# Kernel optimization log

Measured on AMD Instinct MI355X. Metric: run time of the kernel, lower is better.

## Reference

```python
import jax, jax.numpy as jnp
import numpy as np

H = 128          # hidden_size
GRID = 4         # grid_dim
CELL = 0.5       # cell_size
PRED_LEN = 12
EMB = H // 4     # social pooling embed dim = 32


def setup_inputs() -> dict:
    key = jax.random.key(0)
    ks = jax.random.split(key, 13)
    B, N, T = 16384, 64, 8
    s = 0.05
    return {
        "obs": jax.random.normal(ks[0], (B, T, 2), jnp.float32),
        "neighbors": jax.random.normal(ks[1], (B, N, T, 2), jnp.float32),
        "embed_table": jax.random.normal(ks[2], (GRID * GRID + 1, EMB), jnp.float32) * s,
        "W_in": jax.random.normal(ks[3], (H, 2), jnp.float32) * s,
        "b_in": jax.random.normal(ks[4], (H,), jnp.float32) * s,
        "W_sp": jax.random.normal(ks[5], (H, EMB), jnp.float32) * s,
        "b_sp": jax.random.normal(ks[6], (H,), jnp.float32) * s,
        "W_ih": jax.random.normal(ks[7], (4 * H, 2 * H), jnp.float32) * s,
        "W_hh": jax.random.normal(ks[8], (4 * H, H), jnp.float32) * s,
        "b_ih": jax.random.normal(ks[9], (4 * H,), jnp.float32) * s,
        "b_hh": jax.random.normal(ks[10], (4 * H,), jnp.float32) * s,
        "W_out": jax.random.normal(ks[11], (2, H), jnp.float32) * s,
        "b_out": jax.random.normal(ks[12], (2,), jnp.float32) * s,
    }


def reference(obs, neighbors, embed_table, W_in, b_in, W_sp, b_sp,
              W_ih, W_hh, b_ih, b_hh, W_out, b_out):
    B = obs.shape[0]
    half = GRID // 2

    def pool(rel):  # rel: [B, N, 2] -> [B, EMB]
        idx = jnp.clip(jnp.floor(rel / CELL).astype(jnp.int32), -half, half - 1) + half
        # after clamp+shift, idx in [0, GRID-1], so index is always valid (matches torch path)
        flat = idx[..., 0] * GRID + idx[..., 1]  # [B, N]
        return embed_table[flat].sum(axis=1)     # sum-pool over neighbors

    def lstm(h, c, x):  # torch LSTMCell gate order: i, f, g, o
        gates = x @ W_ih.T + b_ih + h @ W_hh.T + b_hh  # [B, 4H]
        i, f, g, o = jnp.split(gates, 4, axis=-1)
        c2 = jax.nn.sigmoid(f) * c + jax.nn.sigmoid(i) * jnp.tanh(g)
        h2 = jax.nn.sigmoid(o) * jnp.tanh(c2)
        return h2, c2

    def obs_step(carry, xs):
        h, c = carry
        o_t, nb_t = xs  # [B,2], [B,N,2]
        agent = o_t @ W_in.T + b_in                        # [B,H]
        social = pool(nb_t - o_t[:, None, :]) @ W_sp.T + b_sp  # [B,H]
        h, c = lstm(h, c, jnp.concatenate([agent, social], axis=-1))
        return (h, c), None

    h0 = jnp.zeros((B, H), obs.dtype)
    c0 = jnp.zeros((B, H), obs.dtype)
    obs_tf = jnp.swapaxes(obs, 0, 1)          # [T,B,2]
    nb_tf = jnp.moveaxis(neighbors, 2, 0)     # [T,B,N,2]
    (h, c), _ = jax.lax.scan(obs_step, (h0, c0), (obs_tf, nb_tf))

    def pred_step(carry, _):
        h, c, prev = carry
        agent = prev @ W_in.T + b_in
        x = jnp.concatenate([agent, jnp.zeros_like(agent)], axis=-1)
        h, c = lstm(h, c, x)
        disp = h @ W_out.T + b_out  # [B,2]
        return (h, c, disp), disp

    prev0 = jnp.zeros((B, 2), obs.dtype)
    _, fut = jax.lax.scan(pred_step, (h, c, prev0), None, length=PRED_LEN)
    return jnp.swapaxes(fut, 0, 1)  # [B, PRED_LEN, 2]
```

## Files before the change

kernel.cpp:

```cpp
#include <hip/hip_runtime.h>
#include <math.h>

typedef _Float16 f16;
typedef f16 f16x8 __attribute__((ext_vector_type(8)));
typedef float f32x4 __attribute__((ext_vector_type(4)));

#define Bsz   16384
#define Tobs  8
#define PREDL 12
#define MR    32

__device__ __forceinline__ float fast_sigm(float x) {
  float e = __builtin_amdgcn_exp2f(-1.44269504f * x);
  return __builtin_amdgcn_rcpf(1.f + e);
}
__device__ __forceinline__ float fast_tanh(float x) {
  float e = __builtin_amdgcn_exp2f(2.88539008f * x);
  return 1.f - 2.f * __builtin_amdgcn_rcpf(1.f + e);
}

#define AB(buf, kt, mt, lane, j) (((((buf)*4 + (kt))*2 + (mt))*64 + (lane))*8 + (j))

#define WF(ktw, w, nt, lane) ((size_t)((((ktw)*8 + (w))*4 + (nt))*64 + (lane)) * 8)

__global__ void wsp_t_kernel(const float* __restrict__ W_sp, const float* __restrict__ table,
                             float* __restrict__ Wsp_t) {
  int gid = blockIdx.x * 256 + threadIdx.x;
  if (gid >= 16 * 128) return;
  int c = gid >> 7, m = gid & 127;
  float s = 0.f;
  for (int e = 0; e < 32; ++e) s += W_sp[m * 32 + e] * table[c * 32 + e];
  Wsp_t[c * 128 + m] = s;
}

__global__ __launch_bounds__(64) void pack_all(
    const float* __restrict__ W_ih, const float* __restrict__ W_hh,
    const float* __restrict__ W_in, const float* __restrict__ Wsp_t,
    const float* __restrict__ b_in, const float* __restrict__ b_sp,
    const float* __restrict__ b_ih, const float* __restrict__ b_hh,
    const float* __restrict__ W_out, const float* __restrict__ b_out,
    f16* __restrict__ Wfrag, float* __restrict__ biasO,
    float* __restrict__ biasP, float* __restrict__ biasPE) {
  const int blk = blockIdx.x;
  const int nt = blk >> 7, w = (blk >> 4) & 7, l = blk & 15;
  const int jo = nt * 128 + w * 16 + l;
  const int m = threadIdx.x;
  __shared__ float st[256];

  float a0 = W_ih[jo * 256 + m],        a1 = W_ih[jo * 256 + 64 + m];
  float s0 = W_ih[jo * 256 + 128 + m],  s1 = W_ih[jo * 256 + 192 + m];
  float hh0 = W_hh[jo * 128 + m],       hh1 = W_hh[jo * 128 + 64 + m];
  float bi0 = b_in[m], bi1 = b_in[64 + m];
  float bs0 = b_sp[m], bs1 = b_sp[64 + m];
  float wi00 = W_in[m * 2 + 0],        wi01 = W_in[m * 2 + 1];
  float wi10 = W_in[(64 + m) * 2 + 0], wi11 = W_in[(64 + m) * 2 + 1];
  float wo00 = W_out[m],       wo01 = W_out[64 + m];
  float wo10 = W_out[128 + m], wo11 = W_out[192 + m];

  auto red = [](float v) {
#pragma unroll
    for (int s = 1; s < 64; s <<= 1) v += __shfl_xor(v, s);
    return v;
  };

  float cells[16];
#pragma unroll
  for (int c = 0; c < 16; ++c)
    cells[c] = red(s0 * Wsp_t[c * 128 + m] + s1 * Wsp_t[c * 128 + 64 + m]);
  float wio0 = red(a0 * wi00 + a1 * wi10);
  float wio1 = red(a0 * wi01 + a1 * wi11);
  float dotA = red(a0 * bi0 + a1 * bi1);
  float dotS = red(s0 * bs0 + s1 * bs1);

  st[m] = hh0;
  st[64 + m] = hh1;
  st[128 + m] = hh0 + wio0 * wo00 + wio1 * wo10;
  st[192 + m] = hh1 + wio0 * wo01 + wio1 * wo11;
  __syncthreads();

  if (m < 32) {
    int u = m & 15, kt = u >> 2, q = u & 3;
    int which = m >> 4;
    int ktw = which ? kt + 5 : kt;
    f16x8 v;
#pragma unroll
    for (int j = 0; j < 8; ++j) v[j] = (f16)st[which * 128 + kt * 32 + q * 8 + j];
    *(f16x8*)(Wfrag + WF(ktw, w, nt, q * 16 + l)) = v;
  } else if (m < 36) {
    int q = m - 32;
    f16x8 v;
#pragma unroll
    for (int j = 0; j < 8; ++j) {
      int kk = q * 8 + j;
      float x = (kk < 16) ? cells[kk] : (kk == 16 ? wio0 : (kk == 17 ? wio1 : 0.f));
      v[j] = (f16)x;
    }
    *(f16x8*)(Wfrag + WF(4, w, nt, q * 16 + l)) = v;
  } else if (m == 36) {
    int col = w * 64 + nt * 16 + l;
    float base = b_ih[jo] + b_hh[jo];
    biasO[col] = base + dotA + dotS;
    float bp = base + dotA;
    biasP[col] = bp;
    biasPE[col] = bp + wio0 * b_out[0] + wio1 * b_out[1];
  }
}

__global__ __launch_bounds__(256) void pool_kernel(const float* __restrict__ obs,
                                                   const float* __restrict__ nb,
                                                   f16* __restrict__ cntx) {
  int tid = threadIdx.x;
  int wv = tid >> 6, ln = tid & 63;
  int b = blockIdx.x * 4 + wv;
  const float4* nb4 = (const float4*)(nb + (((size_t)b * 64 + ln) * 8) * 2);
  float4 n0 = nb4[0], n1 = nb4[1], n2 = nb4[2], n3 = nb4[3];
  const float4* ob4 = (const float4*)(obs + (size_t)b * 16);
  float4 o0 = ob4[0], o1 = ob4[1], o2 = ob4[2], o3 = ob4[3];
  float nxv[8] = {n0.x, n0.z, n1.x, n1.z, n2.x, n2.z, n3.x, n3.z};
  float nyv[8] = {n0.y, n0.w, n1.y, n1.w, n2.y, n2.w, n3.y, n3.w};
  float oxv[8] = {o0.x, o0.z, o1.x, o1.z, o2.x, o2.z, o3.x, o3.z};
  float oyv[8] = {o0.y, o0.w, o1.y, o1.w, o2.y, o2.w, o3.y, o3.w};
  int flat[8];
#pragma unroll
  for (int t = 0; t < 8; ++t) {
    float rx = nxv[t] - oxv[t], ry = nyv[t] - oyv[t];
    int ix = (int)floorf(rx + rx);
    int iy = (int)floorf(ry + ry);
    ix = min(max(ix, -2), 1);
    iy = min(max(iy, -2), 1);
    flat[t] = (ix + 2) * 4 + (iy + 2);
  }
  int cnt0 = 0, cnt1 = 0;
#pragma unroll
  for (int t = 0; t < 8; ++t) {
#pragma unroll
    for (int c = 0; c < 16; ++c) {
      int n = (int)__popcll(__ballot(flat[t] == c));
      if (t < 4) cnt0 = (ln == t * 16 + c) ? n : cnt0;
      else       cnt1 = (ln == (t - 4) * 16 + c) ? n : cnt1;
    }
  }
  int myT = ln >> 4, myC = ln & 15;
  size_t base = (size_t)b * 8;
  cntx[(base + myT) * 32 + myC] = (f16)cnt0;
  cntx[(base + myT + 4) * 32 + myC] = (f16)cnt1;
  if (ln < 8) {
    float ox2 = obs[base * 2 + ln * 2], oy2 = obs[base * 2 + ln * 2 + 1];
    cntx[(base + ln) * 32 + 16] = (f16)ox2;
    cntx[(base + ln) * 32 + 17] = (f16)oy2;
  }
}

__global__ __launch_bounds__(512, 2) void social_lstm_main(
    const f16* __restrict__ Wfrag, const float* __restrict__ biasO,
    const float* __restrict__ biasP, const float* __restrict__ biasPE,
    const f16* __restrict__ cntx, const float* __restrict__ W_out,
    const float* __restrict__ b_out, float* __restrict__ out) {
  __shared__ __align__(16) f16 Abuf[2 * 4 * 2 * 64 * 8];

  const int tid = threadIdx.x;
  const int w = tid >> 6, ln = tid & 63;
  const int q = ln >> 4, l = ln & 15;
  const int b0 = blockIdx.x * MR;

  for (int i = tid; i < 2048; i += 512) ((uint32_t*)Abuf)[i] = 0u;

  f16x8 Bh[4][4];
#pragma unroll
  for (int kt = 0; kt < 4; ++kt)
#pragma unroll
    for (int nt = 0; nt < 4; ++nt)
      Bh[kt][nt] = *(const f16x8*)(Wfrag + WF(kt, w, nt, ln));
  f16x8 Bx[4];
#pragma unroll
  for (int nt = 0; nt < 4; ++nt) Bx[nt] = *(const f16x8*)(Wfrag + WF(4, w, nt, ln));

  float creg[8];
#pragma unroll
  for (int i = 0; i < 8; ++i) creg[i] = 0.f;

  float bOr[4], bPr[4];
#pragma unroll
  for (int g = 0; g < 4; ++g) {
    bOr[g] = biasO[w * 64 + g * 16 + l];
    bPr[g] = biasP[w * 64 + g * 16 + l];
  }

  const int hc = w * 16 + l;
  const int aw_kt = hc >> 5, aw_quad = (hc >> 3) & 3, aw_j = l & 7;

  f32x4 acc[2][4];

  auto gemm_h = [&](int rb) {
#pragma unroll
    for (int kt = 0; kt < 4; ++kt) {
      f16x8 Af[2];
#pragma unroll
      for (int mt = 0; mt < 2; ++mt) Af[mt] = *(const f16x8*)(&Abuf[AB(rb, kt, mt, ln, 0)]);
#pragma unroll
      for (int mt = 0; mt < 2; ++mt)
#pragma unroll
        for (int nt = 0; nt < 4; ++nt)
          acc[mt][nt] =
              __builtin_amdgcn_mfma_f32_16x16x32_f16(Af[mt], Bh[kt][nt], acc[mt][nt], 0, 0, 0);
    }
  };

  auto epilogue = [&](const float* bq, int wbuf) {
#pragma unroll
    for (int mt = 0; mt < 2; ++mt) {
#pragma unroll
      for (int reg = 0; reg < 4; ++reg) {
        float p0 = acc[mt][0][reg] + bq[0];
        float p1 = acc[mt][1][reg] + bq[1];
        float p2 = acc[mt][2][reg] + bq[2];
        float p3 = acc[mt][3][reg] + bq[3];
        float iv = fast_sigm(p0), fv = fast_sigm(p1);
        float gv = fast_tanh(p2), ov = fast_sigm(p3);
        int ci = mt * 4 + reg;
        float c2 = fv * creg[ci] + iv * gv;
        creg[ci] = c2;
        float hv = ov * fast_tanh(c2);
        Abuf[AB(wbuf, aw_kt, mt, (q * 4 + reg) + 16 * aw_quad, aw_j)] = (f16)hv;
      }
    }
  };

#pragma unroll
  for (int t = 0; t < Tobs; ++t) {
    const int rb = t & 1, wb = rb ^ 1;
    __syncthreads();
    f16x8 Ax[2];
#pragma unroll
    for (int mt = 0; mt < 2; ++mt)
      Ax[mt] = *(const f16x8*)(cntx + ((size_t)(b0 + mt * 16 + l) * Tobs + t) * 32 + q * 8);
#pragma unroll
    for (int mt = 0; mt < 2; ++mt)
#pragma unroll
      for (int nt = 0; nt < 4; ++nt) acc[mt][nt] = (f32x4){0.f, 0.f, 0.f, 0.f};
#pragma unroll
    for (int mt = 0; mt < 2; ++mt)
#pragma unroll
      for (int nt = 0; nt < 4; ++nt)
        acc[mt][nt] = __builtin_amdgcn_mfma_f32_16x16x32_f16(Ax[mt], Bx[nt], acc[mt][nt], 0, 0, 0);
    gemm_h(rb);
    epilogue(bOr, wb);
  }

  {
    const int rb = Tobs & 1, wb = rb ^ 1;
    __syncthreads();
#pragma unroll
    for (int mt = 0; mt < 2; ++mt)
#pragma unroll
      for (int nt = 0; nt < 4; ++nt) acc[mt][nt] = (f32x4){0.f, 0.f, 0.f, 0.f};
    gemm_h(rb);
    epilogue(bPr, wb);
  }

#pragma unroll
  for (int kt = 0; kt < 4; ++kt)
#pragma unroll
    for (int nt = 0; nt < 4; ++nt)
      Bh[kt][nt] = *(const f16x8*)(Wfrag + WF(kt + 5, w, nt, ln));
  float bEr[4];
#pragma unroll
  for (int g = 0; g < 4; ++g) bEr[g] = biasPE[w * 64 + g * 16 + l];

  const int d_oi = tid >> 3, d_seg = tid & 7;
  const int d_row = d_oi >> 1, d_jj = d_oi & 1;
  const int d_kt = d_seg >> 1, d_q0 = (d_seg & 1) * 2;
  float wor[16];
  {
    const float4* wp = (const float4*)(W_out + d_jj * 128 + d_seg * 16);
#pragma unroll
    for (int u = 0; u < 4; ++u) {
      float4 v = wp[u];
      wor[4 * u] = v.x; wor[4 * u + 1] = v.y; wor[4 * u + 2] = v.z; wor[4 * u + 3] = v.w;
    }
  }
  const float d_bo = b_out[d_jj];

  auto disp_out = [&](int rbuf, int p) {
    f16x8 hA = *(const f16x8*)(&Abuf[AB(rbuf, d_kt, d_row >> 4, (d_row & 15) + 16 * d_q0, 0)]);
    f16x8 hB = *(const f16x8*)(&Abuf[AB(rbuf, d_kt, d_row >> 4, (d_row & 15) + 16 * (d_q0 + 1), 0)]);
    float s = 0.f;
#pragma unroll
    for (int u = 0; u < 8; ++u) s += wor[u] * (float)hA[u];
#pragma unroll
    for (int u = 0; u < 8; ++u) s += wor[8 + u] * (float)hB[u];
    s += __shfl_xor(s, 1);
    s += __shfl_xor(s, 2);
    s += __shfl_xor(s, 4);
    if ((tid & 7) == 0)
      out[((size_t)(b0 + d_row)) * (PREDL * 2) + p * 2 + d_jj] = s + d_bo;
  };

  for (int p = 1; p < PREDL; ++p) {
    const int s = Tobs + p;
    const int rb = s & 1, wb = rb ^ 1;
    __syncthreads();
    disp_out(rb, p - 1);
#pragma unroll
    for (int mt = 0; mt < 2; ++mt)
#pragma unroll
      for (int nt = 0; nt < 4; ++nt) acc[mt][nt] = (f32x4){0.f, 0.f, 0.f, 0.f};
    gemm_h(rb);
    epilogue(bEr, wb);
  }
  __syncthreads();
  disp_out((Tobs + PREDL) & 1, PREDL - 1);
}

extern "C" void kernel_launch(void* const* d_in, const int* in_sizes, int n_in,
                              void* d_out, int out_size, void* d_ws, size_t ws_size,
                              hipStream_t stream) {
  const float* obs   = (const float*)d_in[0];
  const float* nbrs  = (const float*)d_in[1];
  const float* table = (const float*)d_in[2];
  const float* W_in  = (const float*)d_in[3];
  const float* b_in  = (const float*)d_in[4];
  const float* W_sp  = (const float*)d_in[5];
  const float* b_sp  = (const float*)d_in[6];
  const float* W_ih  = (const float*)d_in[7];
  const float* W_hh  = (const float*)d_in[8];
  const float* b_ih  = (const float*)d_in[9];
  const float* b_hh  = (const float*)d_in[10];
  const float* W_out = (const float*)d_in[11];
  const float* b_out = (const float*)d_in[12];
  float* out = (float*)d_out;

  char* ws = (char*)d_ws;
  f16*   Wfrag  = (f16*)(ws);
  float* biasO  = (float*)(ws + 294912);
  float* biasP  = (float*)(ws + 296960);
  float* biasPE = (float*)(ws + 299008);
  float* Wsp_t  = (float*)(ws + 301056);
  f16*   cntx   = (f16*)(ws + 311296);

  wsp_t_kernel<<<8, 256, 0, stream>>>(W_sp, table, Wsp_t);
  pack_all<<<512, 64, 0, stream>>>(W_ih, W_hh, W_in, Wsp_t, b_in, b_sp, b_ih, b_hh,
                                   W_out, b_out, Wfrag, biasO, biasP, biasPE);
  pool_kernel<<<Bsz / 4, 256, 0, stream>>>(obs, nbrs, cntx);
  social_lstm_main<<<Bsz / MR, 512, 0, stream>>>(Wfrag, biasO, biasP, biasPE, cntx,
                                                 W_out, b_out, out);
}
```

Before: 209.2 us.

## Fuse neighbor pooling into main LSTM kernel and drop Wsp_t precompute kernel

```diff
diff --git a/kernel.cpp b/kernel.cpp
--- a/kernel.cpp
+++ b/kernel.cpp
@@ -20,22 +20,14 @@
 }
 
 #define AB(buf, kt, mt, lane, j) (((((buf)*4 + (kt))*2 + (mt))*64 + (lane))*8 + (j))
+#define CA(t, mt, lane, j) ((((t)*2 + (mt))*64 + (lane))*8 + (j))
 
 #define WF(ktw, w, nt, lane) ((size_t)((((ktw)*8 + (w))*4 + (nt))*64 + (lane)) * 8)
-
-__global__ void wsp_t_kernel(const float* __restrict__ W_sp, const float* __restrict__ table,
-                             float* __restrict__ Wsp_t) {
-  int gid = blockIdx.x * 256 + threadIdx.x;
-  if (gid >= 16 * 128) return;
-  int c = gid >> 7, m = gid & 127;
-  float s = 0.f;
-  for (int e = 0; e < 32; ++e) s += W_sp[m * 32 + e] * table[c * 32 + e];
-  Wsp_t[c * 128 + m] = s;
-}
 
 __global__ __launch_bounds__(64) void pack_all(
     const float* __restrict__ W_ih, const float* __restrict__ W_hh,
-    const float* __restrict__ W_in, const float* __restrict__ Wsp_t,
+    const float* __restrict__ W_in, const float* __restrict__ W_sp,
+    const float* __restrict__ table,
     const float* __restrict__ b_in, const float* __restrict__ b_sp,
     const float* __restrict__ b_ih, const float* __restrict__ b_hh,
     const float* __restrict__ W_out, const float* __restrict__ b_out,
@@ -46,6 +38,8 @@
   const int jo = nt * 128 + w * 16 + l;
   const int m = threadIdx.x;
   __shared__ float st[256];
+  __shared__ float wspPS[32];
+  __shared__ float cellsS[16];
 
   float a0 = W_ih[jo * 256 + m],        a1 = W_ih[jo * 256 + 64 + m];
   float s0 = W_ih[jo * 256 + 128 + m],  s1 = W_ih[jo * 256 + 192 + m];
@@ -63,10 +57,19 @@
     return v;
   };
 
-  float cells[16];
-#pragma unroll
-  for (int c = 0; c < 16; ++c)
-    cells[c] = red(s0 * Wsp_t[c * 128 + m] + s1 * Wsp_t[c * 128 + 64 + m]);
+#pragma unroll 4
+  for (int e = 0; e < 32; ++e) {
+    float wp = red(s0 * W_sp[m * 32 + e] + s1 * W_sp[(64 + m) * 32 + e]);
+    if (m == e) wspPS[e] = wp;
+  }
+  __syncthreads();
+  if (m < 16) {
+    float s = 0.f;
+#pragma unroll
+    for (int e = 0; e < 32; ++e) s += table[m * 32 + e] * wspPS[e];
+    cellsS[m] = s;
+  }
+
   float wio0 = red(a0 * wi00 + a1 * wi10);
   float wio1 = red(a0 * wi01 + a1 * wi11);
   float dotA = red(a0 * bi0 + a1 * bi1);
@@ -92,7 +95,7 @@
 #pragma unroll
     for (int j = 0; j < 8; ++j) {
       int kk = q * 8 + j;
-      float x = (kk < 16) ? cells[kk] : (kk == 16 ? wio0 : (kk == 17 ? wio1 : 0.f));
+      float x = (kk < 16) ? cellsS[kk] : (kk == 16 ? wio0 : (kk == 17 ? wio1 : 0.f));
       v[j] = (f16)x;
     }
     *(f16x8*)(Wfrag + WF(4, w, nt, q * 16 + l)) = v;
@@ -106,57 +109,14 @@
   }
 }
 
-__global__ __launch_bounds__(256) void pool_kernel(const float* __restrict__ obs,
-                                                   const float* __restrict__ nb,
-                                                   f16* __restrict__ cntx) {
-  int tid = threadIdx.x;
-  int wv = tid >> 6, ln = tid & 63;
-  int b = blockIdx.x * 4 + wv;
-  const float4* nb4 = (const float4*)(nb + (((size_t)b * 64 + ln) * 8) * 2);
-  float4 n0 = nb4[0], n1 = nb4[1], n2 = nb4[2], n3 = nb4[3];
-  const float4* ob4 = (const float4*)(obs + (size_t)b * 16);
-  float4 o0 = ob4[0], o1 = ob4[1], o2 = ob4[2], o3 = ob4[3];
-  float nxv[8] = {n0.x, n0.z, n1.x, n1.z, n2.x, n2.z, n3.x, n3.z};
-  float nyv[8] = {n0.y, n0.w, n1.y, n1.w, n2.y, n2.w, n3.y, n3.w};
-  float oxv[8] = {o0.x, o0.z, o1.x, o1.z, o2.x, o2.z, o3.x, o3.z};
-  float oyv[8] = {o0.y, o0.w, o1.y, o1.w, o2.y, o2.w, o3.y, o3.w};
-  int flat[8];
-#pragma unroll
-  for (int t = 0; t < 8; ++t) {
-    float rx = nxv[t] - oxv[t], ry = nyv[t] - oyv[t];
-    int ix = (int)floorf(rx + rx);
-    int iy = (int)floorf(ry + ry);
-    ix = min(max(ix, -2), 1);
-    iy = min(max(iy, -2), 1);
-    flat[t] = (ix + 2) * 4 + (iy + 2);
-  }
-  int cnt0 = 0, cnt1 = 0;
-#pragma unroll
-  for (int t = 0; t < 8; ++t) {
-#pragma unroll
-    for (int c = 0; c < 16; ++c) {
-      int n = (int)__popcll(__ballot(flat[t] == c));
-      if (t < 4) cnt0 = (ln == t * 16 + c) ? n : cnt0;
-      else       cnt1 = (ln == (t - 4) * 16 + c) ? n : cnt1;
-    }
-  }
-  int myT = ln >> 4, myC = ln & 15;
-  size_t base = (size_t)b * 8;
-  cntx[(base + myT) * 32 + myC] = (f16)cnt0;
-  cntx[(base + myT + 4) * 32 + myC] = (f16)cnt1;
-  if (ln < 8) {
-    float ox2 = obs[base * 2 + ln * 2], oy2 = obs[base * 2 + ln * 2 + 1];
-    cntx[(base + ln) * 32 + 16] = (f16)ox2;
-    cntx[(base + ln) * 32 + 17] = (f16)oy2;
-  }
-}
-
 __global__ __launch_bounds__(512, 2) void social_lstm_main(
+    const float* __restrict__ obs, const float* __restrict__ nb,
     const f16* __restrict__ Wfrag, const float* __restrict__ biasO,
     const float* __restrict__ biasP, const float* __restrict__ biasPE,
-    const f16* __restrict__ cntx, const float* __restrict__ W_out,
-    const float* __restrict__ b_out, float* __restrict__ out) {
+    const float* __restrict__ W_out, const float* __restrict__ b_out,
+    float* __restrict__ out) {
   __shared__ __align__(16) f16 Abuf[2 * 4 * 2 * 64 * 8];
+  __shared__ __align__(16) f16 cntA[8 * 2 * 64 * 8];
 
   const int tid = threadIdx.x;
   const int w = tid >> 6, ln = tid & 63;
@@ -164,6 +124,58 @@
   const int b0 = blockIdx.x * MR;
 
   for (int i = tid; i < 2048; i += 512) ((uint32_t*)Abuf)[i] = 0u;
+  for (int i = tid; i < 4096; i += 512) ((uint32_t*)cntA)[i] = 0u;
+  __syncthreads();
+
+  {
+    const int g = ln >> 4, lg = ln & 15;
+    const int r = w * 4 + g;
+    const float4* orow = (const float4*)(obs + (size_t)(b0 + r) * 16);
+    float4 O0 = orow[0], O1 = orow[1], O2 = orow[2], O3 = orow[3];
+    float ox[8] = {O0.x, O0.z, O1.x, O1.z, O2.x, O2.z, O3.x, O3.z};
+    float oy[8] = {O0.y, O0.w, O1.y, O1.w, O2.y, O2.w, O3.y, O3.w};
+    unsigned long long h[8] = {0ull, 0ull, 0ull, 0ull, 0ull, 0ull, 0ull, 0ull};
+#pragma unroll
+    for (int jt = 0; jt < 4; ++jt) {
+      const float4* tr =
+          (const float4*)(nb + ((size_t)(b0 + r) * 64 + (lg + 16 * jt)) * 16);
+      float4 N0 = tr[0], N1 = tr[1], N2 = tr[2], N3 = tr[3];
+      float nx[8] = {N0.x, N0.z, N1.x, N1.z, N2.x, N2.z, N3.x, N3.z};
+      float ny[8] = {N0.y, N0.w, N1.y, N1.w, N2.y, N2.w, N3.y, N3.w};
+#pragma unroll
+      for (int t = 0; t < 8; ++t) {
+        float rx = nx[t] - ox[t], ry = ny[t] - oy[t];
+        int ix = (int)floorf(rx + rx);
+        int iy = (int)floorf(ry + ry);
+        ix = min(max(ix, -2), 1);
+        iy = min(max(iy, -2), 1);
+        int flat = (ix + 2) * 4 + (iy + 2);
+        h[t] += 1ull << (flat * 4);
+      }
+    }
+    auto shx = [](unsigned long long x, int msk) {
+      unsigned lo = __shfl_xor((unsigned)x, msk);
+      unsigned hi = __shfl_xor((unsigned)(x >> 32), msk);
+      return ((unsigned long long)hi << 32) | lo;
+    };
+#pragma unroll
+    for (int t = 0; t < 8; ++t) {
+      unsigned long long v = h[t];
+      v += shx(v, 1);
+      unsigned long long e0 = v & 0x0F0F0F0F0F0F0F0Full;
+      unsigned long long e1 = (v >> 4) & 0x0F0F0F0F0F0F0F0Full;
+      e0 += shx(e0, 2); e1 += shx(e1, 2);
+      e0 += shx(e0, 4); e1 += shx(e1, 4);
+      e0 += shx(e0, 8); e1 += shx(e1, 8);
+      unsigned long long wsel = (lg & 1) ? e1 : e0;
+      unsigned cnt = (unsigned)(wsel >> ((lg >> 1) * 8)) & 0xFFu;
+      cntA[CA(t, r >> 4, (lg >> 3) * 16 + (r & 15), lg & 7)] = (f16)(float)cnt;
+    }
+    int rr = tid >> 4, tt = (tid >> 1) & 7, comp = tid & 1;
+    float xv = obs[(size_t)(b0 + rr) * 16 + tt * 2 + comp];
+    cntA[CA(tt, rr >> 4, 2 * 16 + (rr & 15), comp)] = (f16)xv;
+  }
+  __builtin_amdgcn_sched_barrier(0);
 
   f16x8 Bh[4][4];
 #pragma unroll
@@ -181,15 +193,23 @@
 
   float bOr[4], bPr[4];
 #pragma unroll
-  for (int g = 0; g < 4; ++g) {
-    bOr[g] = biasO[w * 64 + g * 16 + l];
-    bPr[g] = biasP[w * 64 + g * 16 + l];
+  for (int g2 = 0; g2 < 4; ++g2) {
+    bOr[g2] = biasO[w * 64 + g2 * 16 + l];
+    bPr[g2] = biasP[w * 64 + g2 * 16 + l];
   }
 
   const int hc = w * 16 + l;
   const int aw_kt = hc >> 5, aw_quad = (hc >> 3) & 3, aw_j = l & 7;
 
   f32x4 acc[2][4];
+
+  auto acc_init = [&](const float* bq) {
+#pragma unroll
+    for (int mt = 0; mt < 2; ++mt)
+#pragma unroll
+      for (int nt = 0; nt < 4; ++nt)
+        acc[mt][nt] = (f32x4){bq[nt], bq[nt], bq[nt], bq[nt]};
+  };
 
   auto gemm_h = [&](int rb) {
 #pragma unroll
@@ -206,15 +226,15 @@
     }
   };
 
-  auto epilogue = [&](const float* bq, int wbuf) {
+  auto epilogue = [&](int wbuf) {
 #pragma unroll
     for (int mt = 0; mt < 2; ++mt) {
 #pragma unroll
       for (int reg = 0; reg < 4; ++reg) {
-        float p0 = acc[mt][0][reg] + bq[0];
-        float p1 = acc[mt][1][reg] + bq[1];
-        float p2 = acc[mt][2][reg] + bq[2];
-        float p3 = acc[mt][3][reg] + bq[3];
+        float p0 = acc[mt][0][reg];
+        float p1 = acc[mt][1][reg];
+        float p2 = acc[mt][2][reg];
+        float p3 = acc[mt][3][reg];
         float iv = fast_sigm(p0), fv = fast_sigm(p1);
         float gv = fast_tanh(p2), ov = fast_sigm(p3);
         int ci = mt * 4 + reg;
@@ -232,30 +252,23 @@
     __syncthreads();
     f16x8 Ax[2];
 #pragma unroll
-    for (int mt = 0; mt < 2; ++mt)
-      Ax[mt] = *(const f16x8*)(cntx + ((size_t)(b0 + mt * 16 + l) * Tobs + t) * 32 + q * 8);
-#pragma unroll
-    for (int mt = 0; mt < 2; ++mt)
-#pragma unroll
-      for (int nt = 0; nt < 4; ++nt) acc[mt][nt] = (f32x4){0.f, 0.f, 0.f, 0.f};
+    for (int mt = 0; mt < 2; ++mt) Ax[mt] = *(const f16x8*)(&cntA[CA(t, mt, ln, 0)]);
+    acc_init(bOr);
 #pragma unroll
     for (int mt = 0; mt < 2; ++mt)
 #pragma unroll
       for (int nt = 0; nt < 4; ++nt)
         acc[mt][nt] = __builtin_amdgcn_mfma_f32_16x16x32_f16(Ax[mt], Bx[nt], acc[mt][nt], 0, 0, 0);
     gemm_h(rb);
-    epilogue(bOr, wb);
+    epilogue(wb);
   }
 
   {
     const int rb = Tobs & 1, wb = rb ^ 1;
     __syncthreads();
-#pragma unroll
-    for (int mt = 0; mt < 2; ++mt)
-#pragma unroll
-      for (int nt = 0; nt < 4; ++nt) acc[mt][nt] = (f32x4){0.f, 0.f, 0.f, 0.f};
+    acc_init(bPr);
     gemm_h(rb);
-    epilogue(bPr, wb);
+    epilogue(wb);
   }
 
 #pragma unroll
@@ -265,7 +278,7 @@
       Bh[kt][nt] = *(const f16x8*)(Wfrag + WF(kt + 5, w, nt, ln));
   float bEr[4];
 #pragma unroll
-  for (int g = 0; g < 4; ++g) bEr[g] = biasPE[w * 64 + g * 16 + l];
+  for (int g2 = 0; g2 < 4; ++g2) bEr[g2] = biasPE[w * 64 + g2 * 16 + l];
 
   const int d_oi = tid >> 3, d_seg = tid & 7;
   const int d_row = d_oi >> 1, d_jj = d_oi & 1;
@@ -301,12 +314,9 @@
     const int rb = s & 1, wb = rb ^ 1;
     __syncthreads();
     disp_out(rb, p - 1);
-#pragma unroll
-    for (int mt = 0; mt < 2; ++mt)
-#pragma unroll
-      for (int nt = 0; nt < 4; ++nt) acc[mt][nt] = (f32x4){0.f, 0.f, 0.f, 0.f};
+    acc_init(bEr);
     gemm_h(rb);
-    epilogue(bEr, wb);
+    epilogue(wb);
   }
   __syncthreads();
   disp_out((Tobs + PREDL) & 1, PREDL - 1);
@@ -335,13 +345,9 @@
   float* biasO  = (float*)(ws + 294912);
   float* biasP  = (float*)(ws + 296960);
   float* biasPE = (float*)(ws + 299008);
-  float* Wsp_t  = (float*)(ws + 301056);
-  f16*   cntx   = (f16*)(ws + 311296);
-
-  wsp_t_kernel<<<8, 256, 0, stream>>>(W_sp, table, Wsp_t);
-  pack_all<<<512, 64, 0, stream>>>(W_ih, W_hh, W_in, Wsp_t, b_in, b_sp, b_ih, b_hh,
+
+  pack_all<<<512, 64, 0, stream>>>(W_ih, W_hh, W_in, W_sp, table, b_in, b_sp, b_ih, b_hh,
                                    W_out, b_out, Wfrag, biasO, biasP, biasPE);
-  pool_kernel<<<Bsz / 4, 256, 0, stream>>>(obs, nbrs, cntx);
-  social_lstm_main<<<Bsz / MR, 512, 0, stream>>>(Wfrag, biasO, biasP, biasPE, cntx,
+  social_lstm_main<<<Bsz / MR, 512, 0, stream>>>(obs, nbrs, Wfrag, biasO, biasP, biasPE,
                                                  W_out, b_out, out);
 }
```

New measurement: 205.7 us. No clear change (-1.7%).
